# Kernel optimization log

Measured on AMD Instinct MI355X. Metric: run time of the kernel, lower is better.

The kernel has to match this reference:

```python
import jax, jax.numpy as jnp
import numpy as np

N = 25000      # nodes
E = 200000     # edges (avg degree 8)
DIN = 512      # input_dim
HID = 512      # hidden_dim


def setup_inputs() -> dict:
    key = jax.random.key(0)
    ks = jax.random.split(key, 8)
    x = jax.random.normal(ks[0], (N, DIN), jnp.float32)
    edge_index = jax.random.randint(ks[1], (2, E), 0, N, jnp.int32)
    s_in = 1.0 / np.sqrt(DIN).astype(np.float32)
    s_h = 1.0 / np.sqrt(HID).astype(np.float32)
    W1 = jax.random.normal(ks[2], (DIN, HID), jnp.float32) * s_in
    b1 = jnp.zeros((HID,), jnp.float32)
    W2 = jax.random.normal(ks[3], (HID, HID), jnp.float32) * s_h
    b2 = jnp.zeros((HID,), jnp.float32)
    Wo = jax.random.normal(ks[4], (HID, 1), jnp.float32) * s_h
    bo = jnp.zeros((1,), jnp.float32)
    Ww = jax.random.normal(ks[5], (HID, 1), jnp.float32) * s_h
    bw = jnp.zeros((1,), jnp.float32)
    return dict(x=x, edge_index=edge_index, W1=W1, b1=b1, W2=W2, b2=b2,
                Wo=Wo, bo=bo, Ww=Ww, bw=bw)


def reference(x, edge_index, W1, b1, W2, b2, Wo, bo, Ww, bw):
    n = x.shape[0]
    src, dst = edge_index[0], edge_index[1]
    # GCNConv with self-loops: deg counts incoming edges + 1 self-loop
    deg = jax.ops.segment_sum(jnp.ones(src.shape[0], x.dtype), dst,
                              num_segments=n) + 1.0
    dis = jax.lax.rsqrt(deg)              # deg^{-1/2}, [N]
    norm = dis[src] * dis[dst]            # per-edge symmetric norm, [E]

    def gcn(h, W, b):
        hw = h @ W                        # [N, H] dense GEMM
        msg = hw[src] * norm[:, None]     # gather + scale, [E, H]
        agg = jax.ops.segment_sum(msg, dst, num_segments=n)
        agg = agg + hw * (dis * dis)[:, None]  # self-loop contribution
        return agg + b

    h1 = jax.nn.relu(gcn(x, W1, b1))
    h2 = jax.nn.relu(gcn(h1, W2, b2))
    open_logits = (h2 @ Wo + bo)[:, 0]
    wall_logits = (h2 @ Ww + bw)[:, 0]
    return open_logits, wall_logits
```

## Files before the change

### kernel.cpp

```cpp
#include <hip/hip_runtime.h>
#include <hip/hip_bf16.h>

#define DIN 512
#define HID 512

#define AS1 __attribute__((address_space(1)))
#define AS3 __attribute__((address_space(3)))

typedef __attribute__((ext_vector_type(8))) short bfrag;
typedef __attribute__((ext_vector_type(4))) float ffrag;
typedef __attribute__((ext_vector_type(8))) unsigned short u16x8;
typedef __attribute__((ext_vector_type(4))) unsigned short u16x4;


__global__ __launch_bounds__(256) void prelude(const float* __restrict__ x,
                                               unsigned short* __restrict__ xb,
                                               const float* __restrict__ W1,
                                               const float* __restrict__ W2,
                                               unsigned short* __restrict__ Wt1,
                                               unsigned short* __restrict__ Wt2,
                                               const int* __restrict__ dst,
                                               int* __restrict__ cnt,
                                               int E, int Nvalid, int C1) {
    int b = blockIdx.x;
    if (b < C1) {
        int idx = b * 256 + threadIdx.x;
        int row = idx >> 6;
        int c = (idx & 63) * 8;
        unsigned short o[8];
        if (row < Nvalid) {
            float4 a = *(const float4*)&x[(size_t)row * 512 + c];
            float4 v = *(const float4*)&x[(size_t)row * 512 + c + 4];
            __hip_bfloat16 t;
            t = __float2bfloat16(a.x); o[0] = *(unsigned short*)&t;
            t = __float2bfloat16(a.y); o[1] = *(unsigned short*)&t;
            t = __float2bfloat16(a.z); o[2] = *(unsigned short*)&t;
            t = __float2bfloat16(a.w); o[3] = *(unsigned short*)&t;
            t = __float2bfloat16(v.x); o[4] = *(unsigned short*)&t;
            t = __float2bfloat16(v.y); o[5] = *(unsigned short*)&t;
            t = __float2bfloat16(v.z); o[6] = *(unsigned short*)&t;
            t = __float2bfloat16(v.w); o[7] = *(unsigned short*)&t;
        } else {
#pragma unroll
            for (int j = 0; j < 8; ++j) o[j] = 0;
        }
        *(u16x8*)&xb[(size_t)row * 512 + c] = *(u16x8*)o;
    } else if (b < C1 + 512) {
        int bb = b - C1;
        int which = bb >> 8;
        bb &= 255;
        const float* W = which ? W2 : W1;
        unsigned short* Wt = which ? Wt2 : Wt1;
        __shared__ float t[32][33];
        int tid = threadIdx.x;
        int tx = tid & 31, ty = tid >> 5;
        int n0 = (bb & 15) * 32, k0 = (bb >> 4) * 32;
#pragma unroll
        for (int s = 0; s < 4; ++s)
            t[ty + 8 * s][tx] = W[(size_t)(k0 + ty + 8 * s) * 512 + n0 + tx];
        __syncthreads();
#pragma unroll
        for (int s = 0; s < 4; ++s) {
            __hip_bfloat16 v = __float2bfloat16(t[tx][ty + 8 * s]);
            Wt[(size_t)(n0 + ty + 8 * s) * 512 + k0 + tx] = *(unsigned short*)&v;
        }
    } else {
        int e = (b - C1 - 512) * 256 + threadIdx.x;
        if (e < E) atomicAdd(&cnt[dst[e]], 1);
    }
}

__global__ __launch_bounds__(256) void scanA(const int* __restrict__ cnt, int* __restrict__ tmp,
                                             int* __restrict__ bsum, int N) {
    int tid = threadIdx.x, lane = tid & 63, wave = tid >> 6;
    int i = blockIdx.x * 256 + tid;
    int v = (i < N) ? cnt[i] : 0;
    int incl = v;
#pragma unroll
    for (int o = 1; o < 64; o <<= 1) {
        int t = __shfl_up(incl, o);
        if (lane >= o) incl += t;
    }
    __shared__ int wtot[4];
    if (lane == 63) wtot[wave] = incl;
    __syncthreads();
    int woff = 0;
#pragma unroll
    for (int w = 0; w < 4; ++w) woff += (w < wave) ? wtot[w] : 0;
    if (i < N) tmp[i] = woff + incl - v;
    if (tid == 255) bsum[blockIdx.x] = woff + incl;
}

__global__ __launch_bounds__(256) void scanB(const int* __restrict__ cnt,
                                             const int* __restrict__ tmp,
                                             const int* __restrict__ bsum,
                                             int* __restrict__ offs,
                                             int* __restrict__ cursor,
                                             float* __restrict__ dis,
                                             float* __restrict__ out,
                                             const float* __restrict__ bo,
                                             const float* __restrict__ bw,
                                             int N, int nb) {
    int tid = threadIdx.x;
    int lane = tid & 63, wv = tid >> 6;
    int v  = (tid < nb) ? bsum[tid] : 0;
    int vb = (tid < (int)blockIdx.x) ? v : 0;
    int a = v, bfr = vb;
#pragma unroll
    for (int o = 32; o > 0; o >>= 1) {
        a   += __shfl_down(a, o);
        bfr += __shfl_down(bfr, o);
    }
    __shared__ int sa[4], sb[4];
    if (lane == 0) { sa[wv] = a; sb[wv] = bfr; }
    __syncthreads();
    int totalE = sa[0] + sa[1] + sa[2] + sa[3];
    int before = sb[0] + sb[1] + sb[2] + sb[3];

    int i = blockIdx.x * 256 + tid;
    if (i < N) {
        int o = tmp[i] + before;
        offs[i] = o;
        cursor[i] = o;
        int d = cnt[i];
        dis[i] = rsqrtf((float)d + 1.0f);
        out[i] = bo[0];
        out[N + i] = bw[0];
    }
    if (blockIdx.x == 0 && tid == 0) offs[N] = totalE;
}

__device__ inline bool tile_map2(int b, int Mtiles, int& m0, int& n0) {
    int xcd = b & 7, i = b >> 3;
    int nt = i & 1, mg = i >> 1;
    int mt = mg * 8 + xcd;
    if (mt >= Mtiles) return false;
    m0 = mt * 128;
    n0 = nt * 256;
    return true;
}

template <bool ROTA>
__device__ __forceinline__ void gemm_body(const short* __restrict__ A,
                                          const short* __restrict__ B,
                                          unsigned short* __restrict__ C,
                                          int Mtiles, int bidx,
                                          short* As, short* Bs) {
    const int K = 512;
    int m0, n0;
    if (!tile_map2(bidx, Mtiles, m0, n0)) return;
    int tid = threadIdx.x;
    int lane = tid & 63, wave = tid >> 6;
    int wm = (wave & 1) * 64;
    int wn = (wave >> 1) * 128;
    int r = lane & 15, q = lane >> 4;

    unsigned aoff[4]; int aldso[4]; int arow_[4];
#pragma unroll
    for (int i = 0; i < 4; ++i) {
        int s = i * 256 + tid;
        int row = s >> 3;
        int c = (s & 7) ^ (row & 7);
        arow_[i] = m0 + row;
        aoff[i] = (unsigned)(m0 + row) * K + c * 8;
        aldso[i] = (i * 256 + (tid & ~63)) * 8;
    }
    unsigned boff[8]; int bldso[8];
#pragma unroll
    for (int i = 0; i < 8; ++i) {
        int s = i * 256 + tid;
        int row = s >> 3;
        int c = (s & 7) ^ (row & 7);
        boff[i] = (unsigned)(n0 + row) * K + c * 8;
        bldso[i] = (i * 256 + (tid & ~63)) * 8;
    }

    ffrag acc[4][8];
#pragma unroll
    for (int i = 0; i < 4; ++i)
#pragma unroll
        for (int j = 0; j < 8; ++j) acc[i][j] = ffrag{0.f, 0.f, 0.f, 0.f};

    for (int k0 = 0; k0 < K; k0 += 64) {
#pragma unroll
        for (int i = 0; i < 4; ++i) {
            unsigned ka;
            if (ROTA) ka = ((unsigned)(((k0 >> 6) + arow_[i]) & 7)) << 6;
            else ka = (unsigned)k0;
            __builtin_amdgcn_global_load_lds((const AS1 void*)(A + aoff[i] + ka),
                                             (AS3 void*)(As + aldso[i]), 16, 0, 0);
        }
#pragma unroll
        for (int i = 0; i < 8; ++i)
            __builtin_amdgcn_global_load_lds((const AS1 void*)(B + boff[i] + k0),
                                             (AS3 void*)(Bs + bldso[i]), 16, 0, 0);
        __syncthreads();

#pragma unroll
        for (int s2 = 0; s2 < 2; ++s2) {
            bfrag af[4], bfr[8];
#pragma unroll
            for (int i = 0; i < 4; ++i) {
                int arow = wm + i * 16 + r;
                int ach = (s2 * 4 + q) ^ (arow & 7);
                af[i] = *(const bfrag*)&As[arow * 64 + ach * 8];
            }
#pragma unroll
            for (int j = 0; j < 8; ++j) {
                int brow = wn + j * 16 + r;
                int bch = (s2 * 4 + q) ^ (brow & 7);
                bfr[j] = *(const bfrag*)&Bs[brow * 64 + bch * 8];
            }
#pragma unroll
            for (int i = 0; i < 4; ++i)
#pragma unroll
                for (int j = 0; j < 8; ++j)
                    acc[i][j] = __builtin_amdgcn_mfma_f32_16x16x32_bf16(bfr[j], af[i], acc[i][j], 0, 0, 0);
        }
        __syncthreads();
    }

#pragma unroll
    for (int i = 0; i < 4; ++i) {
        int m = m0 + wm + i * 16 + r;
#pragma unroll
        for (int j = 0; j < 8; ++j) {
            int n = n0 + wn + j * 16 + q * 4;
            int np = ((((n >> 6) + m) & 7) << 6) | (n & 63);
            u16x4 o;
#pragma unroll
            for (int reg = 0; reg < 4; ++reg) {
                __hip_bfloat16 v = __float2bfloat16(acc[i][j][reg]);
                o[reg] = *(unsigned short*)&v;
            }
            *(u16x4*)&C[(size_t)m * 512 + np] = o;
        }
    }
}

__global__ __launch_bounds__(256, 2) void gemm_fill(const short* __restrict__ A,
                                                    const short* __restrict__ B,
                                                    unsigned short* __restrict__ C,
                                                    int Mtiles, int G,
                                                    const int* __restrict__ src,
                                                    const int* __restrict__ dst,
                                                    int* __restrict__ cursor,
                                                    const float* __restrict__ dis,
                                                    int2* __restrict__ csr2, int E) {
    __shared__ __align__(16) short As[128 * 64];
    __shared__ __align__(16) short Bs[256 * 64];
    int b = blockIdx.x;
    if (b < G) {
        gemm_body<false>(A, B, C, Mtiles, b, As, Bs);
    } else {
        int e = (b - G) * 256 + threadIdx.x;
        if (e >= E) return;
        int d = dst[e];
        int s = src[e];
        int pos = atomicAdd(&cursor[d], 1);
        int2 rec;
        rec.x = s << 10;
        rec.y = __float_as_int(dis[s] * dis[d]);
        csr2[pos] = rec;
    }
}

__global__ __launch_bounds__(256, 2) void gemm_bf16(const short* __restrict__ A,
                                                    const short* __restrict__ B,
                                                    unsigned short* __restrict__ C,
                                                    int Mtiles) {
    __shared__ __align__(16) short As[128 * 64];
    __shared__ __align__(16) short Bs[256 * 64];
    gemm_body<true>(A, B, C, Mtiles, blockIdx.x, As, Bs);
}

__device__ inline void cvt8(u16x8 v, float* f) {
#pragma unroll
    for (int j = 0; j < 8; ++j) f[j] = __uint_as_float((unsigned)v[j] << 16);
}

__global__ __launch_bounds__(256) void agg_relu_sh(const unsigned short* __restrict__ hw,
                                                   const int2* __restrict__ csr2,
                                                   const int* __restrict__ offs,
                                                   const float* __restrict__ dis,
                                                   const float* __restrict__ bias,
                                                   unsigned short* __restrict__ out,
                                                   int N, int Mpad) {
    int b = blockIdx.x;
    int shard = b & 7;
    int tid = threadIdx.x;
    int wave = tid >> 6, lane = tid & 63;
    int cluster = lane >> 3;
    int sub = lane & 7;
    int node = (b >> 3) * 32 + wave * 8 + cluster;
    int c0 = shard * 64 + sub * 8;
    int sgn = (shard + node) & 7;
    if (node >= N) {
        if (node < Mpad) {
            u16x8 z = {0, 0, 0, 0, 0, 0, 0, 0};
            *(u16x8*)&out[(size_t)node * HID + sgn * 64 + sub * 8] = z;
        }
        return;
    }

    const char* hwb = (const char*)hw + sub * 16;
    float dn = dis[node];
    int e0 = offs[node], e1 = offs[node + 1];

    float acc[8];
    {
        u16x8 sv = *(const u16x8*)(hwb + ((size_t)node << 10) + sgn * 128);
        float g[8];
        cvt8(sv, g);
        float4 bb0 = *(const float4*)&bias[c0];
        float4 bb1 = *(const float4*)&bias[c0 + 4];
        float dis2 = dn * dn;
        acc[0] = g[0] * dis2 + bb0.x; acc[1] = g[1] * dis2 + bb0.y;
        acc[2] = g[2] * dis2 + bb0.z; acc[3] = g[3] * dis2 + bb0.w;
        acc[4] = g[4] * dis2 + bb1.x; acc[5] = g[5] * dis2 + bb1.y;
        acc[6] = g[6] * dis2 + bb1.z; acc[7] = g[7] * dis2 + bb1.w;
    }

    for (int e = e0; e < e1; e += 4) {
        int off[4]; float wgt[4];
#pragma unroll
        for (int t = 0; t < 4; ++t) {
            int ee = e + t;
            int ec = (ee < e1) ? ee : (e1 - 1);
            int2 rec = csr2[ec];
            int sg = (((unsigned)rec.x >> 10) + shard) & 7;
            off[t] = rec.x + sg * 128;
            wgt[t] = (ee < e1) ? __int_as_float(rec.y) : 0.f;
        }
        u16x8 v[4];
#pragma unroll
        for (int t = 0; t < 4; ++t)
            v[t] = *(const u16x8*)(hwb + off[t]);
#pragma unroll
        for (int t = 0; t < 4; ++t) {
            float g[8];
            cvt8(v[t], g);
#pragma unroll
            for (int u = 0; u < 8; ++u) acc[u] += g[u] * wgt[t];
        }
    }

    unsigned short o[8];
#pragma unroll
    for (int t = 0; t < 8; ++t) {
        __hip_bfloat16 v = __float2bfloat16(fmaxf(acc[t], 0.f));
        o[t] = *(unsigned short*)&v;
    }
    *(u16x8*)&out[(size_t)node * HID + sgn * 64 + sub * 8] = *(u16x8*)o;
}

__global__ __launch_bounds__(256) void agg_heads_sh(const unsigned short* __restrict__ hw,
                                                    const int2* __restrict__ csr2,
                                                    const int* __restrict__ offs,
                                                    const float* __restrict__ dis,
                                                    const float* __restrict__ bias,
                                                    const float* __restrict__ Wo,
                                                    const float* __restrict__ Ww,
                                                    float* __restrict__ out, int N) {
    int b = blockIdx.x;
    int shard = b & 7;
    int tid = threadIdx.x;
    int wave = tid >> 6, lane = tid & 63;
    int cluster = lane >> 3;
    int sub = lane & 7;
    int node = (b >> 3) * 32 + wave * 8 + cluster;
    if (node >= N) return;
    int c0 = shard * 64 + sub * 8;
    int sgn = (shard + node) & 7;

    const char* hwb = (const char*)hw + sub * 16;
    float dn = dis[node];
    int e0 = offs[node], e1 = offs[node + 1];

    float acc[8];
    {
        u16x8 sv = *(const u16x8*)(hwb + ((size_t)node << 10) + sgn * 128);
        float g[8];
        cvt8(sv, g);
        float4 bb0 = *(const float4*)&bias[c0];
        float4 bb1 = *(const float4*)&bias[c0 + 4];
        float dis2 = dn * dn;
        acc[0] = g[0] * dis2 + bb0.x; acc[1] = g[1] * dis2 + bb0.y;
        acc[2] = g[2] * dis2 + bb0.z; acc[3] = g[3] * dis2 + bb0.w;
        acc[4] = g[4] * dis2 + bb1.x; acc[5] = g[5] * dis2 + bb1.y;
        acc[6] = g[6] * dis2 + bb1.z; acc[7] = g[7] * dis2 + bb1.w;
    }

    for (int e = e0; e < e1; e += 4) {
        int off[4]; float wgt[4];
#pragma unroll
        for (int t = 0; t < 4; ++t) {
            int ee = e + t;
            int ec = (ee < e1) ? ee : (e1 - 1);
            int2 rec = csr2[ec];
            int sg = (((unsigned)rec.x >> 10) + shard) & 7;
            off[t] = rec.x + sg * 128;
            wgt[t] = (ee < e1) ? __int_as_float(rec.y) : 0.f;
        }
        u16x8 v[4];
#pragma unroll
        for (int t = 0; t < 4; ++t)
            v[t] = *(const u16x8*)(hwb + off[t]);
#pragma unroll
        for (int t = 0; t < 4; ++t) {
            float g[8];
            cvt8(v[t], g);
#pragma unroll
            for (int u = 0; u < 8; ++u) acc[u] += g[u] * wgt[t];
        }
    }

    float4 wo0 = *(const float4*)&Wo[c0];
    float4 wo1 = *(const float4*)&Wo[c0 + 4];
    float4 ww0 = *(const float4*)&Ww[c0];
    float4 ww1 = *(const float4*)&Ww[c0 + 4];
    float po = 0.f, pw = 0.f, h;
    h = fmaxf(acc[0], 0.f); po += h * wo0.x; pw += h * ww0.x;
    h = fmaxf(acc[1], 0.f); po += h * wo0.y; pw += h * ww0.y;
    h = fmaxf(acc[2], 0.f); po += h * wo0.z; pw += h * ww0.z;
    h = fmaxf(acc[3], 0.f); po += h * wo0.w; pw += h * ww0.w;
    h = fmaxf(acc[4], 0.f); po += h * wo1.x; pw += h * ww1.x;
    h = fmaxf(acc[5], 0.f); po += h * wo1.y; pw += h * ww1.y;
    h = fmaxf(acc[6], 0.f); po += h * wo1.z; pw += h * ww1.z;
    h = fmaxf(acc[7], 0.f); po += h * wo1.w; pw += h * ww1.w;

#pragma unroll
    for (int off2 = 4; off2 > 0; off2 >>= 1) {
        po += __shfl_down(po, off2);
        pw += __shfl_down(pw, off2);
    }
    if (sub == 0) {
        atomicAdd(&out[node], po);
        atomicAdd(&out[N + node], pw);
    }
}

extern "C" void kernel_launch(void* const* d_in, const int* in_sizes, int n_in,
                              void* d_out, int out_size, void* d_ws, size_t ws_size,
                              hipStream_t stream) {
    const float* x  = (const float*)d_in[0];
    const int*   ei = (const int*)d_in[1];
    const float* W1 = (const float*)d_in[2];
    const float* b1 = (const float*)d_in[3];
    const float* W2 = (const float*)d_in[4];
    const float* b2 = (const float*)d_in[5];
    const float* Wo = (const float*)d_in[6];
    const float* bo = (const float*)d_in[7];
    const float* Ww = (const float*)d_in[8];
    const float* bw = (const float*)d_in[9];

    const int N = in_sizes[0] / DIN;
    const int E = in_sizes[1] / 2;
    const int Mpad = (N + 127) & ~127;
    const int Mtiles = Mpad / 128;
    const int nb = (N + 255) / 256;
    const int C1 = Mpad / 4;
    const int EJ = (E + 255) / 256;

    char* ws = (char*)d_ws;
    size_t p = 0;
    auto alloc = [&](size_t bytes) -> char* {
        char* r = ws + p;
        p += (bytes + 255) & ~(size_t)255;
        return r;
    };
    int*   cnt    = (int*)alloc((size_t)N * 4);
    int*   offs   = (int*)alloc((size_t)(N + 1) * 4);
    int*   cursor = (int*)alloc((size_t)N * 4);
    int*   tmp    = (int*)alloc((size_t)N * 4);
    int*   bsum   = (int*)alloc(132 * 4);
    float* dis    = (float*)alloc((size_t)N * 4);
    int2*  csr2   = (int2*)alloc((size_t)E * 8 + 64);
    unsigned short* xb  = (unsigned short*)alloc((size_t)Mpad * 512 * 2);
    unsigned short* Wt1 = (unsigned short*)alloc((size_t)512 * 512 * 2);
    unsigned short* Wt2 = (unsigned short*)alloc((size_t)512 * 512 * 2);
    unsigned short* hw  = (unsigned short*)alloc((size_t)Mpad * 512 * 2);
    unsigned short* h1  = (unsigned short*)alloc((size_t)Mpad * 512 * 2);

    const int* src = ei;
    const int* dst = ei + E;

    hipMemsetAsync(cnt, 0, (size_t)N * 4, stream);

    prelude<<<C1 + 512 + EJ, 256, 0, stream>>>(x, xb, W1, W2, Wt1, Wt2,
                                               dst, cnt, E, N, C1);
    scanA<<<nb, 256, 0, stream>>>(cnt, tmp, bsum, N);
    scanB<<<nb, 256, 0, stream>>>(cnt, tmp, bsum, offs, cursor, dis,
                                  (float*)d_out, bo, bw, N, nb);

    const int G = 8 * ((Mtiles + 7) / 8) * 2;
    gemm_fill<<<G + EJ, 256, 0, stream>>>((const short*)xb, (const short*)Wt1, hw,
                                          Mtiles, G, src, dst, cursor, dis, csr2, E);
    agg_relu_sh<<<8 * (Mpad / 32), 256, 0, stream>>>(hw, csr2, offs, dis, b1, h1, N, Mpad);
    gemm_bf16<<<G, 256, 0, stream>>>((const short*)h1, (const short*)Wt2, hw, Mtiles);
    agg_heads_sh<<<8 * ((N + 31) / 32), 256, 0, stream>>>(hw, csr2, offs, dis, b2,
                                                          Wo, Ww, (float*)d_out, N);
}
```

Measured before the change: 222.5 us.

## Sort nodes by in-degree bucket to balance aggregation wave work

```diff
diff --git a/kernel.cpp b/kernel.cpp
--- a/kernel.cpp
+++ b/kernel.cpp
@@ -71,10 +71,12 @@
 }
 
 __global__ __launch_bounds__(256) void scanA(const int* __restrict__ cnt, int* __restrict__ tmp,
-                                             int* __restrict__ bsum, int N) {
+                                             int* __restrict__ bsum, int* __restrict__ hist,
+                                             int N) {
     int tid = threadIdx.x, lane = tid & 63, wave = tid >> 6;
     int i = blockIdx.x * 256 + tid;
     int v = (i < N) ? cnt[i] : 0;
+    if (i < N) atomicAdd(&hist[v > 63 ? 63 : v], 1);
     int incl = v;
 #pragma unroll
     for (int o = 1; o < 64; o <<= 1) {
@@ -94,6 +96,9 @@
 __global__ __launch_bounds__(256) void scanB(const int* __restrict__ cnt,
                                              const int* __restrict__ tmp,
                                              const int* __restrict__ bsum,
+                                             const int* __restrict__ hist,
+                                             int* __restrict__ bcur,
+                                             int* __restrict__ order,
                                              int* __restrict__ offs,
                                              int* __restrict__ cursor,
                                              float* __restrict__ dis,
@@ -102,6 +107,17 @@
                                              const float* __restrict__ bw,
                                              int N, int nb) {
     int tid = threadIdx.x;
+    __shared__ int bb[64];
+    if (tid < 64) {
+        int h = hist[tid];
+        int incl = h;
+#pragma unroll
+        for (int o = 1; o < 64; o <<= 1) {
+            int t = __shfl_up(incl, o);
+            if (tid >= o) incl += t;
+        }
+        bb[tid] = incl - h;
+    }
     int lane = tid & 63, wv = tid >> 6;
     int v  = (tid < nb) ? bsum[tid] : 0;
     int vb = (tid < (int)blockIdx.x) ? v : 0;
@@ -126,6 +142,9 @@
         dis[i] = rsqrtf((float)d + 1.0f);
         out[i] = bo[0];
         out[N + i] = bw[0];
+        int db = d > 63 ? 63 : d;
+        int pos = bb[db] + atomicAdd(&bcur[db], 1);
+        order[pos] = i;
     }
     if (blockIdx.x == 0 && tid == 0) offs[N] = totalE;
 }
@@ -282,6 +301,7 @@
 __global__ __launch_bounds__(256) void agg_relu_sh(const unsigned short* __restrict__ hw,
                                                    const int2* __restrict__ csr2,
                                                    const int* __restrict__ offs,
+                                                   const int* __restrict__ order,
                                                    const float* __restrict__ dis,
                                                    const float* __restrict__ bias,
                                                    unsigned short* __restrict__ out,
@@ -292,7 +312,8 @@
     int wave = tid >> 6, lane = tid & 63;
     int cluster = lane >> 3;
     int sub = lane & 7;
-    int node = (b >> 3) * 32 + wave * 8 + cluster;
+    int idx = (b >> 3) * 32 + wave * 8 + cluster;
+    int node = (idx < N) ? order[idx] : idx;
     int c0 = shard * 64 + sub * 8;
     int sgn = (shard + node) & 7;
     if (node >= N) {
@@ -357,6 +378,7 @@
 __global__ __launch_bounds__(256) void agg_heads_sh(const unsigned short* __restrict__ hw,
                                                     const int2* __restrict__ csr2,
                                                     const int* __restrict__ offs,
+                                                    const int* __restrict__ order,
                                                     const float* __restrict__ dis,
                                                     const float* __restrict__ bias,
                                                     const float* __restrict__ Wo,
@@ -368,8 +390,9 @@
     int wave = tid >> 6, lane = tid & 63;
     int cluster = lane >> 3;
     int sub = lane & 7;
-    int node = (b >> 3) * 32 + wave * 8 + cluster;
-    if (node >= N) return;
+    int idx = (b >> 3) * 32 + wave * 8 + cluster;
+    if (idx >= N) return;
+    int node = order[idx];
     int c0 = shard * 64 + sub * 8;
     int sgn = (shard + node) & 7;
 
@@ -469,11 +492,14 @@
         p += (bytes + 255) & ~(size_t)255;
         return r;
     };
-    int*   cnt    = (int*)alloc((size_t)N * 4);
+    int*   cnt    = (int*)alloc((size_t)(N + 128) * 4);
+    int*   hist   = cnt + N;
+    int*   bcur   = cnt + N + 64;
     int*   offs   = (int*)alloc((size_t)(N + 1) * 4);
     int*   cursor = (int*)alloc((size_t)N * 4);
     int*   tmp    = (int*)alloc((size_t)N * 4);
     int*   bsum   = (int*)alloc(132 * 4);
+    int*   order  = (int*)alloc((size_t)N * 4);
     float* dis    = (float*)alloc((size_t)N * 4);
     int2*  csr2   = (int2*)alloc((size_t)E * 8 + 64);
     unsigned short* xb  = (unsigned short*)alloc((size_t)Mpad * 512 * 2);
@@ -485,19 +511,19 @@
     const int* src = ei;
     const int* dst = ei + E;
 
-    hipMemsetAsync(cnt, 0, (size_t)N * 4, stream);
+    hipMemsetAsync(cnt, 0, (size_t)(N + 128) * 4, stream);
 
     prelude<<<C1 + 512 + EJ, 256, 0, stream>>>(x, xb, W1, W2, Wt1, Wt2,
                                                dst, cnt, E, N, C1);
-    scanA<<<nb, 256, 0, stream>>>(cnt, tmp, bsum, N);
-    scanB<<<nb, 256, 0, stream>>>(cnt, tmp, bsum, offs, cursor, dis,
+    scanA<<<nb, 256, 0, stream>>>(cnt, tmp, bsum, hist, N);
+    scanB<<<nb, 256, 0, stream>>>(cnt, tmp, bsum, hist, bcur, order, offs, cursor, dis,
                                   (float*)d_out, bo, bw, N, nb);
 
     const int G = 8 * ((Mtiles + 7) / 8) * 2;
     gemm_fill<<<G + EJ, 256, 0, stream>>>((const short*)xb, (const short*)Wt1, hw,
                                           Mtiles, G, src, dst, cursor, dis, csr2, E);
-    agg_relu_sh<<<8 * (Mpad / 32), 256, 0, stream>>>(hw, csr2, offs, dis, b1, h1, N, Mpad);
+    agg_relu_sh<<<8 * (Mpad / 32), 256, 0, stream>>>(hw, csr2, offs, order, dis, b1, h1, N, Mpad);
     gemm_bf16<<<G, 256, 0, stream>>>((const short*)h1, (const short*)Wt2, hw, Mtiles);
-    agg_heads_sh<<<8 * ((N + 31) / 32), 256, 0, stream>>>(hw, csr2, offs, dis, b2,
+    agg_heads_sh<<<8 * ((N + 31) / 32), 256, 0, stream>>>(hw, csr2, offs, order, dis, b2,
                                                           Wo, Ww, (float*)d_out, N);
 }
```

Measured after the change: 373.5 us. 1.68x slower.
